# Kernel tuning notes

Hardware: AMD Instinct MI355X
Metric: run time of the kernel (lower is better)

Reference implementation:

```python
import jax, jax.numpy as jnp
import numpy as np

N = 10000      # nodes of this type
T = 160000     # total metapath instances (ragged rows)
D = 256        # input_dim
P = 256        # pre_embed_dim
H = 512        # mlp_settings['layer_list'][0]
S = 64         # select_dim


def setup_inputs() -> dict:
    key = jax.random.key(0)
    ks = jax.random.split(key, 16)
    def w(k, shape):
        return jax.random.normal(k, shape, jnp.float32) / np.sqrt(shape[0]).astype(np.float32)
    return {
        "feat_A": jax.random.normal(ks[0], (N, D), jnp.float32),
        "feat_AP": jax.random.normal(ks[1], (T, D), jnp.float32),
        "feat_APA": jax.random.normal(ks[2], (T, 2 * D), jnp.float32),
        "seg_AP": jnp.sort(jax.random.randint(ks[3], (T,), 0, N, jnp.int32)),
        "seg_APA": jnp.sort(jax.random.randint(ks[4], (T,), 0, N, jnp.int32)),
        "type_weight": w(ks[5], (D, P)),
        "W_enc_AP": w(ks[6], (D, H)),   "b_enc_AP": jnp.zeros((H,), jnp.float32),
        "W_dec_AP": w(ks[7], (H, P)),   "b_dec_AP": jnp.zeros((P,), jnp.float32),
        "W_enc_APA": w(ks[8], (2 * D, H)), "b_enc_APA": jnp.zeros((H,), jnp.float32),
        "W_dec_APA": w(ks[9], (H, P)),  "b_dec_APA": jnp.zeros((P,), jnp.float32),
        "W_attn1": w(ks[10], (2 * P, 2 * P)),
        "W_attn2": w(ks[11], (2 * P, 1)),
        "W_cls": w(ks[12], (P, S)), "b_cls": jnp.zeros((S,), jnp.float32),
    }


def reference(feat_A, feat_AP, feat_APA, seg_AP, seg_APA, type_weight,
              W_enc_AP, b_enc_AP, W_dec_AP, b_dec_AP,
              W_enc_APA, b_enc_APA, W_dec_APA, b_dec_APA,
              W_attn1, W_attn2, W_cls, b_cls):
    # center node embedding (metapath of length 1): feat @ type_weight
    center = feat_A @ type_weight                                  # [N, P]

    def metapath_path(feat, seg, We, be, Wd, bd):
        # per-metapath MLP encode (Linear+ReLU) / decode (Linear)
        h = jax.nn.relu(feat @ We + be)                            # [T, H]
        dec = h @ Wd + bd                                          # [T, P]
        # ragged split + per-node sum aggregation; empty segments -> zeros
        return jax.ops.segment_sum(dec, seg, num_segments=N,
                                   indices_are_sorted=True)        # [N, P]

    inj_AP = metapath_path(feat_AP, seg_AP, W_enc_AP, b_enc_AP, W_dec_AP, b_dec_AP)
    inj_APA = metapath_path(feat_APA, seg_APA, W_enc_APA, b_enc_APA, W_dec_APA, b_dec_APA)

    def attn_score(inj):
        # attn = Tanh -> Linear(2P,2P,no bias) -> Linear(2P,1,no bias) -> LeakyReLU(0.1), then mean
        x = jnp.tanh(jnp.concatenate([center, inj], axis=1))       # [N, 2P]
        s = (x @ W_attn1) @ W_attn2                                # [N, 1]
        return jax.nn.leaky_relu(s, 0.1).mean()

    # index 0 corresponds to the length-1 metapath (never scored; fixed to 0)
    scores = jnp.stack([jnp.zeros((), jnp.float32), attn_score(inj_AP), attn_score(inj_APA)])
    wts = jax.nn.softmax(scores)                                   # [3]

    inj_AP = inj_AP * wts[1]
    inj_APA = inj_APA * wts[2]
    embed = (inj_AP + inj_APA) * 0.5                               # stack(...,dim=2).mean(dim=2)
    pre_embed = jax.nn.log_softmax((center + embed) @ W_cls + b_cls, axis=1)  # [N, S]
    return pre_embed, inj_AP, inj_APA
```

## Files before the change

### kernel.cpp

```cpp
#include <hip/hip_runtime.h>
#include <stdint.h>

typedef __bf16 bf16x8 __attribute__((ext_vector_type(8)));
typedef __bf16 bf16x4 __attribute__((ext_vector_type(4)));
typedef float  f32x4  __attribute__((ext_vector_type(4)));

#define N_NODES 10000
#define T_ROWS  160000
#define HDIM    512
#define PDIM    256

__device__ __forceinline__ f32x4 mfma16(bf16x8 a, bf16x8 b, f32x4 c) {
    return __builtin_amdgcn_mfma_f32_16x16x32_bf16(a, b, c, 0, 0, 0);
}

__device__ __forceinline__ void pack_one(const float* __restrict__ W,
                                         __bf16* __restrict__ out,
                                         int K, int Nc, int ltid) {
    int lane = ltid & 63;
    int t = ltid >> 6;
    int KT = K >> 5;
    int kt = t % KT, nt = t / KT;
    int col = (nt << 4) + (lane & 15);
    int krow = (kt << 5) + ((lane >> 4) << 3);
    __bf16* dst = out + ((size_t)ltid << 3);
#pragma unroll
    for (int e = 0; e < 8; ++e)
        dst[e] = (__bf16)W[(size_t)(krow + e) * Nc + col];
}

__global__ void pack5_kernel(
    const float* __restrict__ tw,    __bf16* __restrict__ twP,
    const float* __restrict__ WeAP,  __bf16* __restrict__ WeAPp,
    const float* __restrict__ WdAP,  __bf16* __restrict__ WdAPp,
    const float* __restrict__ WeAPA, __bf16* __restrict__ WeAPAp,
    const float* __restrict__ WdAPA, __bf16* __restrict__ WdAPAp)
{
    int tid = blockIdx.x * 256 + threadIdx.x;
    if      (tid <  8192) pack_one(tw,    twP,    256, 256, tid);
    else if (tid < 24576) pack_one(WeAP,  WeAPp,  256, 512, tid - 8192);
    else if (tid < 40960) pack_one(WdAP,  WdAPp,  512, 256, tid - 24576);
    else if (tid < 73728) pack_one(WeAPA, WeAPAp, 512, 512, tid - 40960);
    else if (tid < 90112) pack_one(WdAPA, WdAPAp, 512, 256, tid - 73728);
}

template<int DIN>
__device__ __forceinline__ void path_body(
    const float* __restrict__ X,
    const __bf16* __restrict__ WeP, const float* __restrict__ be,
    const __bf16* __restrict__ WdP, const float* __restrict__ bd,
    const int* __restrict__ seg,
    float* __restrict__ inj,
    int tile, __bf16* buf, int* segs)
{
    constexpr int LDX = DIN + 8;
    constexpr int LDH = HDIM + 8;
    constexpr int KT1 = DIN / 32;
    const int tid = threadIdx.x;
    const int row0 = tile * 64;
    if (tid < 64) segs[tid] = seg[row0 + tid];

#pragma unroll 4
    for (int i = tid; i < 64 * (DIN / 4); i += 512) {
        int r = i / (DIN / 4), c4 = i % (DIN / 4);
        float4 f = ((const float4*)X)[(size_t)(row0 + r) * (DIN / 4) + c4];
        bf16x4 h;
        h[0] = (__bf16)f.x; h[1] = (__bf16)f.y; h[2] = (__bf16)f.z; h[3] = (__bf16)f.w;
        *(bf16x4*)&buf[r * LDX + c4 * 4] = h;
    }
    __syncthreads();

    const int wave = tid >> 6, lane = tid & 63;
    const int lr = lane & 15, lg = lane >> 4;

    f32x4 acc1[4][4] = {};
    {
        const __bf16* w1 = WeP + ((size_t)(wave * 4) * KT1) * 512 + lane * 8;
        bf16x8 bX[4], bY[4], a[4];
#pragma unroll
        for (int ct = 0; ct < 4; ++ct) bX[ct] = *(const bf16x8*)&w1[(size_t)(ct * KT1) * 512];
        for (int kt = 0; kt < KT1; kt += 2) {
#pragma unroll
            for (int ct = 0; ct < 4; ++ct)
                bY[ct] = *(const bf16x8*)&w1[(size_t)(ct * KT1 + kt + 1) * 512];
            int ko = kt * 32 + lg * 8;
#pragma unroll
            for (int rt = 0; rt < 4; ++rt)
                a[rt] = *(const bf16x8*)&buf[(rt * 16 + lr) * LDX + ko];
            __builtin_amdgcn_s_setprio(1);
#pragma unroll
            for (int ct = 0; ct < 4; ++ct)
#pragma unroll
                for (int rt = 0; rt < 4; ++rt)
                    acc1[rt][ct] = mfma16(a[rt], bX[ct], acc1[rt][ct]);
            __builtin_amdgcn_s_setprio(0);
            int kn = (kt + 2 < KT1) ? kt + 2 : 0;
#pragma unroll
            for (int ct = 0; ct < 4; ++ct)
                bX[ct] = *(const bf16x8*)&w1[(size_t)(ct * KT1 + kn) * 512];
            ko = (kt + 1) * 32 + lg * 8;
#pragma unroll
            for (int rt = 0; rt < 4; ++rt)
                a[rt] = *(const bf16x8*)&buf[(rt * 16 + lr) * LDX + ko];
            __builtin_amdgcn_s_setprio(1);
#pragma unroll
            for (int ct = 0; ct < 4; ++ct)
#pragma unroll
                for (int rt = 0; rt < 4; ++rt)
                    acc1[rt][ct] = mfma16(a[rt], bY[ct], acc1[rt][ct]);
            __builtin_amdgcn_s_setprio(0);
        }
    }
    __syncthreads();

#pragma unroll
    for (int ct = 0; ct < 4; ++ct) {
        int col = wave * 64 + ct * 16 + lr;
        float bias = be[col];
#pragma unroll
        for (int rt = 0; rt < 4; ++rt) {
            int rbase = rt * 16 + lg * 4;
#pragma unroll
            for (int j = 0; j < 4; ++j) {
                float vl = acc1[rt][ct][j] + bias;
                buf[(rbase + j) * LDH + col] = (__bf16)(vl > 0.f ? vl : 0.f);
            }
        }
    }
    __syncthreads();

    f32x4 acc2[4][2] = {};
    {
        const __bf16* w2 = WdP + ((size_t)(wave * 2) * 16) * 512 + lane * 8;
        bf16x8 bX2[2], bY2[2], aX[4], aY[4];
#pragma unroll
        for (int ct = 0; ct < 2; ++ct) bX2[ct] = *(const bf16x8*)&w2[(size_t)(ct * 16) * 512];
#pragma unroll
        for (int rt = 0; rt < 4; ++rt)
            aX[rt] = *(const bf16x8*)&buf[(rt * 16 + lr) * LDH + lg * 8];
        for (int kt = 0; kt < 16; kt += 2) {
#pragma unroll
            for (int ct = 0; ct < 2; ++ct)
                bY2[ct] = *(const bf16x8*)&w2[(size_t)(ct * 16 + kt + 1) * 512];
            int ko = (kt + 1) * 32 + lg * 8;
#pragma unroll
            for (int rt = 0; rt < 4; ++rt)
                aY[rt] = *(const bf16x8*)&buf[(rt * 16 + lr) * LDH + ko];
            __builtin_amdgcn_s_setprio(1);
#pragma unroll
            for (int ct = 0; ct < 2; ++ct)
#pragma unroll
                for (int rt = 0; rt < 4; ++rt)
                    acc2[rt][ct] = mfma16(aX[rt], bX2[ct], acc2[rt][ct]);
            __builtin_amdgcn_s_setprio(0);
            int kn = (kt + 2 < 16) ? kt + 2 : 0;
#pragma unroll
            for (int ct = 0; ct < 2; ++ct)
                bX2[ct] = *(const bf16x8*)&w2[(size_t)(ct * 16 + kn) * 512];
            ko = kn * 32 + lg * 8;
#pragma unroll
            for (int rt = 0; rt < 4; ++rt)
                aX[rt] = *(const bf16x8*)&buf[(rt * 16 + lr) * LDH + ko];
            __builtin_amdgcn_s_setprio(1);
#pragma unroll
            for (int ct = 0; ct < 2; ++ct)
#pragma unroll
                for (int rt = 0; rt < 4; ++rt)
                    acc2[rt][ct] = mfma16(aY[rt], bY2[ct], acc2[rt][ct]);
            __builtin_amdgcn_s_setprio(0);
        }
    }
#pragma unroll
    for (int ct = 0; ct < 2; ++ct) {
        int col = wave * 32 + ct * 16 + lr;
        float bias = bd[col];
#pragma unroll
        for (int rt = 0; rt < 4; ++rt) {
            int rbase = rt * 16 + lg * 4;
            float run = acc2[rt][ct][0] + bias;
            int cur = segs[rbase];
#pragma unroll
            for (int j = 1; j < 4; ++j) {
                float vl = acc2[rt][ct][j] + bias;
                int s = segs[rbase + j];
                if (s == cur) run += vl;
                else {
                    atomicAdd(&inj[(size_t)cur * PDIM + col], run);
                    cur = s; run = vl;
                }
            }
            atomicAdd(&inj[(size_t)cur * PDIM + col], run);
        }
    }
}

__global__ __launch_bounds__(512, 4) void paths_kernel(
    const float* __restrict__ featAP,  const float* __restrict__ featAPA,
    const __bf16* __restrict__ WeAPp,  const float* __restrict__ beAP,
    const __bf16* __restrict__ WdAPp,  const float* __restrict__ bdAP,
    const __bf16* __restrict__ WeAPAp, const float* __restrict__ beAPA,
    const __bf16* __restrict__ WdAPAp, const float* __restrict__ bdAPA,
    const int* __restrict__ segAP, const int* __restrict__ segAPA,
    float* __restrict__ injAP, float* __restrict__ injAPA)
{
    __shared__ __bf16 buf[64 * (HDIM + 8)];
    __shared__ int segs[64];
    int bid = blockIdx.x;
    int p = bid >> 1;
    int tile = (p & 3) * 625 + (p >> 2);
    if (bid & 1)
        path_body<512>(featAPA, WeAPAp, beAPA, WdAPAp, bdAPA, segAPA, injAPA,
                       tile, buf, segs);
    else
        path_body<256>(featAP, WeAPp, beAP, WdAPp, bdAP, segAP, injAP,
                       tile, buf, segs);
}

__global__ __launch_bounds__(512, 4) void center_kernel(
    const float* __restrict__ feat, const __bf16* __restrict__ twP,
    float* __restrict__ center)
{
    constexpr int LDX = 264;
    __shared__ __bf16 xs[64 * LDX];
    const int tid = threadIdx.x;
    const int row0 = blockIdx.x * 64;
#pragma unroll 4
    for (int i = tid; i < 64 * 64; i += 512) {
        int r = i / 64, c4 = i % 64;
        int row = row0 + r;
        float4 f = {0.f, 0.f, 0.f, 0.f};
        if (row < N_NODES) f = ((const float4*)feat)[(size_t)row * 64 + c4];
        bf16x4 h;
        h[0] = (__bf16)f.x; h[1] = (__bf16)f.y; h[2] = (__bf16)f.z; h[3] = (__bf16)f.w;
        *(bf16x4*)&xs[r * LDX + c4 * 4] = h;
    }
    __syncthreads();

    const int wave = tid >> 6, lane = tid & 63;
    const int lr = lane & 15, lg = lane >> 4;
    f32x4 acc[4][2] = {};
    const __bf16* w = twP + ((size_t)(wave * 2) * 8) * 512 + lane * 8;
    for (int kt = 0; kt < 8; ++kt) {
        int ko = kt * 32 + lg * 8;
        bf16x8 a[4];
#pragma unroll
        for (int rt = 0; rt < 4; ++rt)
            a[rt] = *(const bf16x8*)&xs[(rt * 16 + lr) * LDX + ko];
#pragma unroll
        for (int ct = 0; ct < 2; ++ct) {
            bf16x8 b = *(const bf16x8*)&w[(size_t)(ct * 8 + kt) * 512];
#pragma unroll
            for (int rt = 0; rt < 4; ++rt)
                acc[rt][ct] = mfma16(a[rt], b, acc[rt][ct]);
        }
    }
#pragma unroll
    for (int ct = 0; ct < 2; ++ct) {
        int col = wave * 32 + ct * 16 + lr;
#pragma unroll
        for (int rt = 0; rt < 4; ++rt) {
            int rbase = rt * 16 + lg * 4;
#pragma unroll
            for (int j = 0; j < 4; ++j) {
                int row = row0 + rbase + j;
                if (row < N_NODES) center[(size_t)row * 256 + col] = acc[rt][ct][j];
            }
        }
    }
}

__global__ void attn_v_kernel(const float* __restrict__ W1, const float* __restrict__ W2,
                              float* __restrict__ v) {
    int k = threadIdx.x;
    float s = 0.f;
    for (int j = 0; j < 512; ++j) s += W1[k * 512 + j] * W2[j];
    v[k] = s;
}

__global__ __launch_bounds__(256, 4) void score2_kernel(
    const float* __restrict__ center, const float* __restrict__ injAP,
    const float* __restrict__ injAPA, const float* __restrict__ v,
    float* __restrict__ sacc)
{
    const int w = threadIdx.x >> 6, lane = threadIdx.x & 63;
    float l1 = 0.f, l2 = 0.f;
    for (int row = blockIdx.x * 4 + w; row < N_NODES; row += gridDim.x * 4) {
        float x1 = 0.f, x2 = 0.f;
#pragma unroll
        for (int k = 0; k < 4; ++k) {
            int c = lane + k * 64;
            size_t off = (size_t)row * 256 + c;
            float tc = tanhf(center[off]) * v[c];
            float vi = v[256 + c];
            x1 += tc + tanhf(injAP[off]) * vi;
            x2 += tc + tanhf(injAPA[off]) * vi;
        }
#pragma unroll
        for (int o = 32; o > 0; o >>= 1) {
            x1 += __shfl_xor(x1, o);
            x2 += __shfl_xor(x2, o);
        }
        if (lane == 0) {
            l1 += (x1 > 0.f) ? x1 : 0.1f * x1;
            l2 += (x2 > 0.f) ? x2 : 0.1f * x2;
        }
    }
    if (lane == 0) {
        atomicAdd(&sacc[0], l1);
        atomicAdd(&sacc[1], l2);
    }
}

__global__ __launch_bounds__(256, 4) void final_kernel(
    const float* __restrict__ center, const float* __restrict__ injAP,
    const float* __restrict__ injAPA, const float* __restrict__ sacc,
    const float* __restrict__ Wcls, const float* __restrict__ bcls,
    float* __restrict__ out0, float* __restrict__ out1, float* __restrict__ out2)
{
    __shared__ float zs[4][256];
    float s1 = sacc[0] * (1.f / N_NODES), s2 = sacc[1] * (1.f / N_NODES);
    float m0 = fmaxf(0.f, fmaxf(s1, s2));
    float e0 = expf(0.f - m0), e1 = expf(s1 - m0), e2 = expf(s2 - m0);
    float inv = 1.f / (e0 + e1 + e2);
    const float w1 = e1 * inv, w2 = e2 * inv;

    const int row0 = blockIdx.x * 4;
    for (int idx = threadIdx.x; idx < 1024; idx += 256) {
        int r = idx >> 8, c = idx & 255;
        size_t off = (size_t)(row0 + r) * 256 + c;
        float a = injAP[off] * w1, b = injAPA[off] * w2;
        out1[off] = a; out2[off] = b;
        zs[r][c] = center[off] + 0.5f * (a + b);
    }
    __syncthreads();
    const int g = threadIdx.x >> 6, j = threadIdx.x & 63;
    float logit = bcls[j];
    for (int k = 0; k < 256; ++k) logit += zs[g][k] * Wcls[k * 64 + j];
    float m = logit;
#pragma unroll
    for (int o = 32; o > 0; o >>= 1) m = fmaxf(m, __shfl_xor(m, o));
    float e = expf(logit - m);
    float se = e;
#pragma unroll
    for (int o = 32; o > 0; o >>= 1) se += __shfl_xor(se, o);
    out0[(size_t)(row0 + g) * 64 + j] = (logit - m) - logf(se);
}

extern "C" void kernel_launch(void* const* d_in, const int* in_sizes, int n_in,
                              void* d_out, int out_size, void* d_ws, size_t ws_size,
                              hipStream_t stream)
{
    const float* feat_A   = (const float*)d_in[0];
    const float* feat_AP  = (const float*)d_in[1];
    const float* feat_APA = (const float*)d_in[2];
    const int*   seg_AP   = (const int*)d_in[3];
    const int*   seg_APA  = (const int*)d_in[4];
    const float* type_w   = (const float*)d_in[5];
    const float* We_AP    = (const float*)d_in[6];
    const float* be_AP    = (const float*)d_in[7];
    const float* Wd_AP    = (const float*)d_in[8];
    const float* bd_AP    = (const float*)d_in[9];
    const float* We_APA   = (const float*)d_in[10];
    const float* be_APA   = (const float*)d_in[11];
    const float* Wd_APA   = (const float*)d_in[12];
    const float* bd_APA   = (const float*)d_in[13];
    const float* W_attn1  = (const float*)d_in[14];
    const float* W_attn2  = (const float*)d_in[15];
    const float* W_cls    = (const float*)d_in[16];
    const float* b_cls    = (const float*)d_in[17];

    char* ws = (char*)d_ws;
    size_t o = 0;
    auto alloc = [&](size_t bytes) { char* p = ws + o; o += (bytes + 255) & ~size_t(255); return p; };
    float* center = (float*)alloc((size_t)N_NODES * 256 * 4);
    float* injAP  = (float*)alloc((size_t)N_NODES * 256 * 4);
    float* injAPA = (float*)alloc((size_t)N_NODES * 256 * 4);
    float* vbuf   = (float*)alloc(512 * 4);
    float* sacc   = (float*)alloc(256);
    __bf16* twP    = (__bf16*)alloc(256 * 256 * 2);
    __bf16* WeAPp  = (__bf16*)alloc(256 * 512 * 2);
    __bf16* WdAPp  = (__bf16*)alloc(512 * 256 * 2);
    __bf16* WeAPAp = (__bf16*)alloc(512 * 512 * 2);
    __bf16* WdAPAp = (__bf16*)alloc(512 * 256 * 2);

    hipMemsetAsync(injAP,  0, (size_t)N_NODES * 256 * 4, stream);
    hipMemsetAsync(injAPA, 0, (size_t)N_NODES * 256 * 4, stream);
    hipMemsetAsync(sacc,   0, 256, stream);

    pack5_kernel<<<352, 256, 0, stream>>>(type_w, twP, We_AP, WeAPp, Wd_AP, WdAPp,
                                          We_APA, WeAPAp, Wd_APA, WdAPAp);
    attn_v_kernel<<<1, 512, 0, stream>>>(W_attn1, W_attn2, vbuf);
    center_kernel<<<(N_NODES + 63) / 64, 512, 0, stream>>>(feat_A, twP, center);
    paths_kernel<<<2 * (T_ROWS / 64), 512, 0, stream>>>(
        feat_AP, feat_APA, WeAPp, be_AP, WdAPp, bd_AP,
        WeAPAp, be_APA, WdAPAp, bd_APA, seg_AP, seg_APA, injAP, injAPA);
    score2_kernel<<<256, 256, 0, stream>>>(center, injAP, injAPA, vbuf, sacc);

    float* out0 = (float*)d_out;
    float* out1 = out0 + (size_t)N_NODES * 64;
    float* out2 = out1 + (size_t)N_NODES * 256;
    final_kernel<<<N_NODES / 4, 256, 0, stream>>>(center, injAP, injAPA, sacc,
                                                  W_cls, b_cls, out0, out1, out2);
}
```

Measured before the change: 489.6 us.

## Stage decoder output in LDS and reduce segments per column before atomics

The decoder accumulators are written to shared memory, and each thread then scans 32 consecutive rows of one column, summing runs of equal segment ids. Segments that lie entirely inside the 32-row slice are written with plain stores; only the boundary runs use atomicAdd. This cuts global atomic traffic, which was previously one atomic per 4-row fragment. The tile order is also changed to sequential, so neighbouring tiles run close together in time. The cost is two extra barriers and an LDS round trip. The plain stores assume no other slice touches that segment, which holds only because the segment array is sorted.

Result: faster. 427.9 us (-12.6%).

```diff
diff --git a/kernel.cpp b/kernel.cpp
--- a/kernel.cpp
+++ b/kernel.cpp
@@ -55,6 +55,7 @@
 {
     constexpr int LDX = DIN + 8;
     constexpr int LDH = HDIM + 8;
+    constexpr int LDP = 260;
     constexpr int KT1 = DIN / 32;
     const int tid = threadIdx.x;
     const int row0 = tile * 64;
@@ -170,6 +171,9 @@
             __builtin_amdgcn_s_setprio(0);
         }
     }
+    __syncthreads();
+
+    float* decs = (float*)buf;
 #pragma unroll
     for (int ct = 0; ct < 2; ++ct) {
         int col = wave * 32 + ct * 16 + lr;
@@ -177,20 +181,31 @@
 #pragma unroll
         for (int rt = 0; rt < 4; ++rt) {
             int rbase = rt * 16 + lg * 4;
-            float run = acc2[rt][ct][0] + bias;
-            int cur = segs[rbase];
-#pragma unroll
-            for (int j = 1; j < 4; ++j) {
-                float vl = acc2[rt][ct][j] + bias;
-                int s = segs[rbase + j];
-                if (s == cur) run += vl;
-                else {
-                    atomicAdd(&inj[(size_t)cur * PDIM + col], run);
-                    cur = s; run = vl;
-                }
+#pragma unroll
+            for (int j = 0; j < 4; ++j)
+                decs[(rbase + j) * LDP + col] = acc2[rt][ct][j] + bias;
+        }
+    }
+    __syncthreads();
+
+    {
+        const int c  = wave * 32 + (lane & 31);
+        const int rs = (lane >> 5) * 32;
+        float run = decs[rs * LDP + c];
+        int cur = segs[rs];
+        int runstart = rs;
+#pragma unroll
+        for (int r = rs + 1; r < rs + 32; ++r) {
+            int s = segs[r];
+            float v = decs[r * LDP + c];
+            if (s == cur) run += v;
+            else {
+                if (runstart != rs) inj[(size_t)cur * PDIM + c] = run;
+                else atomicAdd(&inj[(size_t)cur * PDIM + c], run);
+                cur = s; run = v; runstart = r;
             }
-            atomicAdd(&inj[(size_t)cur * PDIM + col], run);
-        }
+        }
+        atomicAdd(&inj[(size_t)cur * PDIM + c], run);
     }
 }
 
@@ -206,8 +221,7 @@
     __shared__ __bf16 buf[64 * (HDIM + 8)];
     __shared__ int segs[64];
     int bid = blockIdx.x;
-    int p = bid >> 1;
-    int tile = (p & 3) * 625 + (p >> 2);
+    int tile = bid >> 1;
     if (bid & 1)
         path_body<512>(featAPA, WeAPAp, beAPA, WdAPAp, bdAPA, segAPA, injAPA,
                        tile, buf, segs);
```
